# Kernel tuning notes

Hardware: AMD Instinct MI355X
Metric: run time of the kernel (lower is better)

The kernel has to match this reference:

```python
import jax, jax.numpy as jnp
from jax import lax
import numpy as np

T, B, I, H = 2048, 64, 256, 256  # time-major LSTM, standard 4H gate layout


def setup_inputs() -> dict:
    key = jax.random.key(0)
    k = jax.random.split(key, 5)
    s = 1.0 / np.sqrt(H)
    return {
        "x": jax.random.normal(k[0], (T, B, I), dtype=jnp.float32),
        "W_ih": jax.random.uniform(k[1], (4 * H, I), jnp.float32, -s, s),
        "W_hh": jax.random.uniform(k[2], (4 * H, H), jnp.float32, -s, s),
        "b_ih": jax.random.uniform(k[3], (4 * H,), jnp.float32, -s, s),
        "b_hh": jax.random.uniform(k[4], (4 * H,), jnp.float32, -s, s),
    }


def reference(x, W_ih, W_hh, b_ih, b_hh):
    # Precompute input projections for all timesteps in one big GEMM: [T, B, 4H]
    x_proj = jnp.einsum("tbi,gi->tbg", x, W_ih) + b_ih + b_hh

    def step(carry, xp_t):
        h, c = carry
        gates = xp_t + h @ W_hh.T  # [B, 4H]
        i, f, g, o = jnp.split(gates, 4, axis=-1)
        c = jax.nn.sigmoid(f) * c + jax.nn.sigmoid(i) * jnp.tanh(g)
        h = jax.nn.sigmoid(o) * jnp.tanh(c)
        return (h, c), None

    init = (jnp.zeros((x.shape[1], H), x.dtype), jnp.zeros((x.shape[1], H), x.dtype))
    (h_last, c_last), _ = lax.scan(step, init, x_proj)
    # torch loop overwrites `outputs` each step and returns only the final h
    return h_last
```

## Files before the change

kernel.cpp:

```cpp
#include <hip/hip_runtime.h>
#include <hip/hip_bf16.h>
#include <stdint.h>


#define T_STEPS 2048
#define NWG 32

typedef float f32x4 __attribute__((ext_vector_type(4)));
typedef short bf16x8 __attribute__((ext_vector_type(8)));
typedef uint32_t u32x4 __attribute__((ext_vector_type(4)));

__device__ __forceinline__ short tobf(float f) {
    __hip_bfloat16 h = __float2bfloat16(f);
    return *reinterpret_cast<short*>(&h);
}

__device__ __forceinline__ bf16x8 pack8(f32x4 a, f32x4 b) {
    bf16x8 r;
    r[0] = tobf(a[0]); r[1] = tobf(a[1]); r[2] = tobf(a[2]); r[3] = tobf(a[3]);
    r[4] = tobf(b[0]); r[5] = tobf(b[1]); r[6] = tobf(b[2]); r[7] = tobf(b[3]);
    return r;
}

__device__ __forceinline__ bf16x8 frag_u64(unsigned long long a, unsigned long long b) {
    u32x4 t;
    t.x = (uint32_t)a; t.y = (uint32_t)(a >> 32);
    t.z = (uint32_t)b; t.w = (uint32_t)(b >> 32);
    return __builtin_bit_cast(bf16x8, t);
}

__device__ __forceinline__ float fast_sig(float x) {
    float e = __builtin_amdgcn_exp2f(-1.4426950408889634f * x);
    return __builtin_amdgcn_rcpf(1.0f + e);
}
__device__ __forceinline__ float fast_tanh(float x) {
    float xc = fminf(fmaxf(x, -15.0f), 15.0f);
    float e = __builtin_amdgcn_exp2f(2.8853900817779268f * xc);
    return (e - 1.0f) * __builtin_amdgcn_rcpf(e + 1.0f);
}

__global__ __launch_bounds__(256, 1)
void lstm_fused(const float* __restrict__ x,
                const float* __restrict__ W_ih,
                const float* __restrict__ W_hh,
                const float* __restrict__ b_ih,
                const float* __restrict__ b_hh,
                float* __restrict__ out,
                uint32_t* __restrict__ hbuf,
                uint32_t* __restrict__ flags)
{
    const int wg   = blockIdx.x;
    const int tid  = threadIdx.x;
    const int wv   = tid >> 6;
    const int l    = tid & 63;
    const int l15  = l & 15;
    const int lk   = l >> 4;
    const int gate = l15 >> 2;
    const int jj   = l15 & 3;

    bf16x8 wf[2][16];
    float bias[2];
#pragma unroll
    for (int p = 0; p < 2; ++p) {
        const int grow = 256 * gate + 8 * wg + 4 * p + jj;
#pragma unroll
        for (int kt = 0; kt < 16; ++kt) {
            const float* src = (kt < 8)
                ? (W_ih + (size_t)grow * 256 + kt * 32 + lk * 8)
                : (W_hh + (size_t)grow * 256 + (kt - 8) * 32 + lk * 8);
            wf[p][kt] = pack8(*(const f32x4*)(src), *(const f32x4*)(src + 4));
        }
        bias[p] = b_ih[grow] + b_hh[grow];
    }

    const int arow = 16 * wv + l15;
    const float* xbase = x + (size_t)arow * 256 + lk * 8;

    float cst[2][4] = {{0.f,0.f,0.f,0.f},{0.f,0.f,0.f,0.f}};

    f32x4 xs[16];
#pragma unroll
    for (int kt = 0; kt < 8; ++kt) {
        xs[2 * kt]     = *(const f32x4*)(xbase + kt * 32);
        xs[2 * kt + 1] = *(const f32x4*)(xbase + kt * 32 + 4);
    }

    for (int s = 0; s < T_STEPS; ++s) {
        if (s > 0 && tid < 64) {
            const uint32_t target = (uint32_t)s;
            const uint32_t* fp = flags + (l & (NWG - 1)) * 16;
            while (true) {
                uint32_t v = __hip_atomic_load(fp, __ATOMIC_RELAXED, __HIP_MEMORY_SCOPE_AGENT);
                if (__all((int)(v >= target))) break;
                __builtin_amdgcn_s_sleep(1);
            }
        }
        __syncthreads();
        asm volatile("" ::: "memory");

        const unsigned long long* hb = (const unsigned long long*)
            (hbuf + (size_t)(s & 1) * 8192 + (size_t)arow * 128 + 4 * lk);
        unsigned long long hq[16];
#pragma unroll
        for (int kh = 0; kh < 8; ++kh) {
            hq[2 * kh]     = __hip_atomic_load(hb + (size_t)kh * 8,
                                               __ATOMIC_RELAXED, __HIP_MEMORY_SCOPE_AGENT);
            hq[2 * kh + 1] = __hip_atomic_load(hb + (size_t)kh * 8 + 1,
                                               __ATOMIC_RELAXED, __HIP_MEMORY_SCOPE_AGENT);
        }

        bf16x8 af[8];
#pragma unroll
        for (int kt = 0; kt < 8; ++kt) af[kt] = pack8(xs[2 * kt], xs[2 * kt + 1]);

        f32x4 aA[2] = {{0.f,0.f,0.f,0.f},{0.f,0.f,0.f,0.f}};
        f32x4 aB[2] = {{0.f,0.f,0.f,0.f},{0.f,0.f,0.f,0.f}};
#pragma unroll
        for (int kt = 0; kt < 8; kt += 2) {
#pragma unroll
            for (int p = 0; p < 2; ++p) {
                aA[p] = __builtin_amdgcn_mfma_f32_16x16x32_bf16(af[kt],     wf[p][kt],     aA[p], 0, 0, 0);
                aB[p] = __builtin_amdgcn_mfma_f32_16x16x32_bf16(af[kt + 1], wf[p][kt + 1], aB[p], 0, 0, 0);
            }
        }

        if (s + 1 < T_STEPS) {
            const float* xp = xbase + (size_t)(s + 1) * 16384;
#pragma unroll
            for (int kt = 0; kt < 8; ++kt) {
                xs[2 * kt]     = *(const f32x4*)(xp + kt * 32);
                xs[2 * kt + 1] = *(const f32x4*)(xp + kt * 32 + 4);
            }
        }

#pragma unroll
        for (int kh = 0; kh < 8; kh += 2) {
            bf16x8 h0 = frag_u64(hq[2 * kh],     hq[2 * kh + 1]);
            bf16x8 h1 = frag_u64(hq[2 * kh + 2], hq[2 * kh + 3]);
#pragma unroll
            for (int p = 0; p < 2; ++p) {
                aA[p] = __builtin_amdgcn_mfma_f32_16x16x32_bf16(h0, wf[p][8 + kh],     aA[p], 0, 0, 0);
                aB[p] = __builtin_amdgcn_mfma_f32_16x16x32_bf16(h1, wf[p][8 + kh + 1], aB[p], 0, 0, 0);
            }
        }

        uint32_t* hw_out = hbuf + (size_t)((s + 1) & 1) * 8192;
        const int orow0 = 16 * wv + 4 * lk;
        float hv[2][4];
#pragma unroll
        for (int p = 0; p < 2; ++p) {
#pragma unroll
            for (int r = 0; r < 4; ++r) {
                float vo  = aA[p][r] + aB[p][r] + bias[p];
                float v4  = __shfl_xor(vo, 4);
                float v8  = __shfl_xor(vo, 8);
                float v12 = __shfl_xor(vo, 12);
                float iv = (gate == 0) ? vo : ((gate == 1) ? v4 : ((gate == 2) ? v8 : v12));
                float fv = (gate == 1) ? vo : ((gate == 0) ? v4 : ((gate == 3) ? v8 : v12));
                float gv = (gate == 2) ? vo : ((gate == 3) ? v4 : ((gate == 0) ? v8 : v12));
                float ov = (gate == 3) ? vo : ((gate == 2) ? v4 : ((gate == 1) ? v8 : v12));
                float cn = fast_sig(fv) * cst[p][r] + fast_sig(iv) * fast_tanh(gv);
                cst[p][r] = cn;
                hv[p][r] = fast_sig(ov) * fast_tanh(cn);
            }
        }

#pragma unroll
        for (int p = 0; p < 2; ++p) {
#pragma unroll
            for (int r = 0; r < 4; ++r) {
                uint32_t hu = (uint32_t)(uint16_t)tobf(hv[p][r]);
                uint32_t pu = (uint32_t)__shfl_xor((int)hu, 1);
                uint32_t packed = hu | (pu << 16);
                if ((l & 13) == 0) {
                    __hip_atomic_store(hw_out + (size_t)(orow0 + r) * 128
                                           + 4 * wg + 2 * p + (jj >> 1),
                                       packed, __ATOMIC_RELAXED, __HIP_MEMORY_SCOPE_AGENT);
                }
            }
        }

        if (s == T_STEPS - 1) {
#pragma unroll
            for (int p = 0; p < 2; ++p)
#pragma unroll
                for (int r = 0; r < 4; ++r)
                    if ((l & 12) == 0)
                        out[(size_t)(orow0 + r) * 256 + 8 * wg + 4 * p + jj] = hv[p][r];
        }

        __syncthreads();
        if (tid == 0)
            __hip_atomic_store(flags + wg * 16, (uint32_t)(s + 1),
                               __ATOMIC_RELEASE, __HIP_MEMORY_SCOPE_AGENT);
    }
}

extern "C" void kernel_launch(void* const* d_in, const int* in_sizes, int n_in,
                              void* d_out, int out_size, void* d_ws, size_t ws_size,
                              hipStream_t stream) {
    const float* x    = (const float*)d_in[0];
    const float* W_ih = (const float*)d_in[1];
    const float* W_hh = (const float*)d_in[2];
    const float* b_ih = (const float*)d_in[3];
    const float* b_hh = (const float*)d_in[4];
    float* out = (float*)d_out;

    uint32_t* hbuf  = (uint32_t*)d_ws;
    uint32_t* flags = hbuf + 2 * 8192;

    hipMemsetAsync(d_ws, 0, (2 * 8192 + NWG * 16) * sizeof(uint32_t), stream);

    lstm_fused<<<dim3(NWG), dim3(256), 0, stream>>>(x, W_ih, W_hh, b_ih, b_hh,
                                                    out, hbuf, flags);
}
```

Before: 12.87 ms.

## Use per-wave flags and move next-step input projection off the critical path

```diff
diff --git a/kernel.cpp b/kernel.cpp
--- a/kernel.cpp
+++ b/kernel.cpp
@@ -84,18 +84,40 @@
         xs[2 * kt]     = *(const f32x4*)(xbase + kt * 32);
         xs[2 * kt + 1] = *(const f32x4*)(xbase + kt * 32 + 4);
     }
+    f32x4 aA[2] = {{0.f,0.f,0.f,0.f},{0.f,0.f,0.f,0.f}};
+    f32x4 aB[2] = {{0.f,0.f,0.f,0.f},{0.f,0.f,0.f,0.f}};
+    {
+        bf16x8 af[8];
+#pragma unroll
+        for (int kt = 0; kt < 8; ++kt) af[kt] = pack8(xs[2 * kt], xs[2 * kt + 1]);
+#pragma unroll
+        for (int kt = 0; kt < 8; kt += 2)
+#pragma unroll
+            for (int p = 0; p < 2; ++p) {
+                aA[p] = __builtin_amdgcn_mfma_f32_16x16x32_bf16(af[kt],     wf[p][kt],     aA[p], 0, 0, 0);
+                aB[p] = __builtin_amdgcn_mfma_f32_16x16x32_bf16(af[kt + 1], wf[p][kt + 1], aB[p], 0, 0, 0);
+            }
+#pragma unroll
+        for (int kt = 0; kt < 8; ++kt) {
+            const float* p1 = xbase + 16384 + kt * 32;
+            xs[2 * kt]     = *(const f32x4*)(p1);
+            xs[2 * kt + 1] = *(const f32x4*)(p1 + 4);
+        }
+    }
+
+    const uint32_t* mypollline = flags + wv * 32 + (l & 31);
+    uint32_t* myflag = flags + wv * 32 + wg;
 
     for (int s = 0; s < T_STEPS; ++s) {
-        if (s > 0 && tid < 64) {
+        if (s > 0) {
             const uint32_t target = (uint32_t)s;
-            const uint32_t* fp = flags + (l & (NWG - 1)) * 16;
             while (true) {
-                uint32_t v = __hip_atomic_load(fp, __ATOMIC_RELAXED, __HIP_MEMORY_SCOPE_AGENT);
+                uint32_t v = __hip_atomic_load(mypollline, __ATOMIC_RELAXED,
+                                               __HIP_MEMORY_SCOPE_AGENT);
                 if (__all((int)(v >= target))) break;
                 __builtin_amdgcn_s_sleep(1);
             }
         }
-        __syncthreads();
         asm volatile("" ::: "memory");
 
         const unsigned long long* hb = (const unsigned long long*)
@@ -107,30 +129,6 @@
                                                __ATOMIC_RELAXED, __HIP_MEMORY_SCOPE_AGENT);
             hq[2 * kh + 1] = __hip_atomic_load(hb + (size_t)kh * 8 + 1,
                                                __ATOMIC_RELAXED, __HIP_MEMORY_SCOPE_AGENT);
-        }
-
-        bf16x8 af[8];
-#pragma unroll
-        for (int kt = 0; kt < 8; ++kt) af[kt] = pack8(xs[2 * kt], xs[2 * kt + 1]);
-
-        f32x4 aA[2] = {{0.f,0.f,0.f,0.f},{0.f,0.f,0.f,0.f}};
-        f32x4 aB[2] = {{0.f,0.f,0.f,0.f},{0.f,0.f,0.f,0.f}};
-#pragma unroll
-        for (int kt = 0; kt < 8; kt += 2) {
-#pragma unroll
-            for (int p = 0; p < 2; ++p) {
-                aA[p] = __builtin_amdgcn_mfma_f32_16x16x32_bf16(af[kt],     wf[p][kt],     aA[p], 0, 0, 0);
-                aB[p] = __builtin_amdgcn_mfma_f32_16x16x32_bf16(af[kt + 1], wf[p][kt + 1], aB[p], 0, 0, 0);
-            }
-        }
-
-        if (s + 1 < T_STEPS) {
-            const float* xp = xbase + (size_t)(s + 1) * 16384;
-#pragma unroll
-            for (int kt = 0; kt < 8; ++kt) {
-                xs[2 * kt]     = *(const f32x4*)(xp + kt * 32);
-                xs[2 * kt + 1] = *(const f32x4*)(xp + kt * 32 + 4);
-            }
         }
 
 #pragma unroll
@@ -189,10 +187,32 @@
                         out[(size_t)(orow0 + r) * 256 + 8 * wg + 4 * p + jj] = hv[p][r];
         }
 
-        __syncthreads();
-        if (tid == 0)
-            __hip_atomic_store(flags + wg * 16, (uint32_t)(s + 1),
+        if (l == 0)
+            __hip_atomic_store(myflag, (uint32_t)(s + 1),
                                __ATOMIC_RELEASE, __HIP_MEMORY_SCOPE_AGENT);
+
+        if (s + 1 < T_STEPS) {
+            bf16x8 af[8];
+#pragma unroll
+            for (int kt = 0; kt < 8; ++kt) af[kt] = pack8(xs[2 * kt], xs[2 * kt + 1]);
+#pragma unroll
+            for (int p = 0; p < 2; ++p) { aA[p] = (f32x4){0.f,0.f,0.f,0.f}; aB[p] = (f32x4){0.f,0.f,0.f,0.f}; }
+#pragma unroll
+            for (int kt = 0; kt < 8; kt += 2)
+#pragma unroll
+                for (int p = 0; p < 2; ++p) {
+                    aA[p] = __builtin_amdgcn_mfma_f32_16x16x32_bf16(af[kt],     wf[p][kt],     aA[p], 0, 0, 0);
+                    aB[p] = __builtin_amdgcn_mfma_f32_16x16x32_bf16(af[kt + 1], wf[p][kt + 1], aB[p], 0, 0, 0);
+                }
+            if (s + 2 < T_STEPS) {
+                const float* xp = xbase + (size_t)(s + 2) * 16384;
+#pragma unroll
+                for (int kt = 0; kt < 8; ++kt) {
+                    xs[2 * kt]     = *(const f32x4*)(xp + kt * 32);
+                    xs[2 * kt + 1] = *(const f32x4*)(xp + kt * 32 + 4);
+                }
+            }
+        }
     }
 }
 
@@ -209,7 +229,7 @@
     uint32_t* hbuf  = (uint32_t*)d_ws;
     uint32_t* flags = hbuf + 2 * 8192;
 
-    hipMemsetAsync(d_ws, 0, (2 * 8192 + NWG * 16) * sizeof(uint32_t), stream);
+    hipMemsetAsync(d_ws, 0, (2 * 8192 + 4 * 32) * sizeof(uint32_t), stream);
 
     lstm_fused<<<dim3(NWG), dim3(256), 0, stream>>>(x, W_ih, W_hh, b_ih, b_hh,
                                                     out, hbuf, flags);
```

Result: slower. 13.96 ms (+8.5%).
